# Optimization experiments

Hardware: AMD Instinct MI355X
Metric: run time of the kernel (lower is better)

The kernel has to match this reference:

```python
import jax, jax.numpy as jnp
import numpy as np

N_HEADS = 8
D_EMBED = 1024
D_CROSS = 768
D_HEAD = D_EMBED // N_HEADS  # 128; used only as softmax scale (matches original code)


def setup_inputs() -> dict:
    key = jax.random.key(0)
    ks = jax.random.split(key, 10)
    B, Lq, Lkv = 16, 4096, 77
    s_e = 1.0 / np.sqrt(D_EMBED)
    s_c = 1.0 / np.sqrt(D_CROSS)
    return {
        "x": jax.random.normal(ks[0], (B, Lq, D_EMBED), jnp.float32),
        "y": jax.random.normal(ks[1], (B, Lkv, D_CROSS), jnp.float32),
        "Wq": jax.random.normal(ks[2], (D_EMBED, D_EMBED), jnp.float32) * s_e,
        "bq": jnp.zeros((D_EMBED,), jnp.float32),
        "Wk": jax.random.normal(ks[3], (D_CROSS, D_EMBED), jnp.float32) * s_c,
        "bk": jnp.zeros((D_EMBED,), jnp.float32),
        "Wv": jax.random.normal(ks[4], (D_CROSS, D_EMBED), jnp.float32) * s_c,
        "bv": jnp.zeros((D_EMBED,), jnp.float32),
        "Wo": jax.random.normal(ks[5], (D_EMBED, D_EMBED), jnp.float32) * s_e,
        "bo": jnp.zeros((D_EMBED,), jnp.float32),
    }


def reference(x, y, Wq, bq, Wk, bk, Wv, bv, Wo, bo):
    # Projections
    q = jnp.einsum("bqd,de->bqe", x, Wq) + bq          # [B, Lq, D]
    k = jnp.einsum("bkc,ce->bke", y, Wk) + bk          # [B, Lkv, D]
    v = jnp.einsum("bkc,ce->bke", y, Wv) + bv          # [B, Lkv, D]
    # Original module does NOT split heads; scale uses d_head = d_embed // n_heads
    scale = 1.0 / np.sqrt(D_HEAD)
    scores = jnp.einsum("bqe,bke->bqk", q, k) * scale  # [B, Lq, Lkv]
    attn = jax.nn.softmax(scores, axis=-1)
    out = jnp.einsum("bqk,bke->bqe", attn, v)          # [B, Lq, D]
    return jnp.einsum("bqe,ef->bqf", out, Wo) + bo
```

## Files before the change

### kernel.cpp

```cpp
#include <hip/hip_runtime.h>

typedef unsigned short u16;
typedef __bf16 bf16x8 __attribute__((ext_vector_type(8)));
typedef float f32x4 __attribute__((ext_vector_type(4)));

static __device__ __forceinline__ u16 f2bf(float f) {
  unsigned u = __builtin_bit_cast(unsigned, f);
  u = u + 0x7FFFu + ((u >> 16) & 1u);
  return (u16)(u >> 16);
}
static __device__ __forceinline__ float bf2f(u16 h) {
  return __builtin_bit_cast(float, (unsigned)h << 16);
}

#define GLOAD_LDS16(g, l) __builtin_amdgcn_global_load_lds(              \
    (const __attribute__((address_space(1))) void*)(g),                  \
    (__attribute__((address_space(3))) void*)(l), 16, 0, 0)
#define BAR() asm volatile("s_barrier" ::: "memory")
#define VMCNT(n) asm volatile("s_waitcnt vmcnt(" #n ")" ::: "memory")
#define LGKM0() do { asm volatile("s_waitcnt lgkmcnt(0)" ::: "memory");   \
                     __builtin_amdgcn_sched_barrier(0); } while (0)

__global__ __launch_bounds__(256) void prep(
    const float* __restrict__ Wq, const float* __restrict__ bq,
    const float* __restrict__ Wk, const float* __restrict__ bk,
    const float* __restrict__ Wv, const float* __restrict__ bv,
    const float* __restrict__ Wo, const float* __restrict__ y,
    u16* __restrict__ Wqb, u16* __restrict__ Wkb, u16* __restrict__ Wvb,
    u16* __restrict__ Wot, u16* __restrict__ yp,
    float* __restrict__ zeros, float* __restrict__ bvo,
    float* __restrict__ wkbq, float* __restrict__ bkq) {
  __shared__ float tile[32][33];
  const int blk = blockIdx.x, tid = threadIdx.x;
  if (blk < 4) {
    zeros[blk * 256 + tid] = 0.f;
  } else if (blk < 8) {
    int j = (blk - 4) * 256 + tid;
    float s = 0.f;
    for (int e = 0; e < 1024; ++e) s += bv[e] * Wo[(long)e * 1024 + j];
    bvo[j] = s;
  } else if (blk < 200) {
    int w = (blk - 8) * 4 + (tid >> 6);
    int lane = tid & 63;
    const float* r = Wk + (long)w * 1024;
    float s = 0.f;
#pragma unroll
    for (int i = 0; i < 4; ++i) {
      f32x4 a = *reinterpret_cast<const f32x4*>(r + lane * 4 + i * 256);
      f32x4 b = *reinterpret_cast<const f32x4*>(bq + lane * 4 + i * 256);
      s += a[0] * b[0] + a[1] * b[1] + a[2] * b[2] + a[3] * b[3];
    }
#pragma unroll
    for (int off = 1; off < 64; off <<= 1) s += __shfl_xor(s, off, 64);
    if (lane == 0) wkbq[w] = s;
  } else if (blk < 456) {
    int w = (blk - 200) * 4 + (tid >> 6);
    int lane = tid & 63;
    const float* r = Wq + (long)w * 1024;
    float s = 0.f;
#pragma unroll
    for (int i = 0; i < 4; ++i) {
      f32x4 a = *reinterpret_cast<const f32x4*>(r + lane * 4 + i * 256);
      f32x4 b = *reinterpret_cast<const f32x4*>(bk + lane * 4 + i * 256);
      s += a[0] * b[0] + a[1] * b[1] + a[2] * b[2] + a[3] * b[3];
    }
#pragma unroll
    for (int off = 1; off < 64; off <<= 1) s += __shfl_xor(s, off, 64);
    if (lane == 0) bkq[w] = s;
  } else if (blk < 3016) {
    const float* src; u16* dst; long i;
    if (blk < 1480)      { src = Wq; dst = Wqb; i = (long)(blk - 456) * 256 + tid; }
    else if (blk < 2248) { src = Wk; dst = Wkb; i = (long)(blk - 1480) * 256 + tid; }
    else                 { src = Wv; dst = Wvb; i = (long)(blk - 2248) * 256 + tid; }
    float4 v = reinterpret_cast<const float4*>(src)[i];
    ushort4 o;
    o.x = f2bf(v.x); o.y = f2bf(v.y); o.z = f2bf(v.z); o.w = f2bf(v.w);
    reinterpret_cast<ushort4*>(dst)[i] = o;
  } else if (blk < 4040) {
    int lb = blk - 3016;
    const int tx = tid & 31, ty = tid >> 5;
    const int n0 = (lb & 31) * 32, k0 = (lb >> 5) * 32;
#pragma unroll
    for (int i = 0; i < 4; ++i)
      tile[ty + i * 8][tx] = Wo[(long)(k0 + ty + i * 8) * 1024 + n0 + tx];
    __syncthreads();
#pragma unroll
    for (int i = 0; i < 4; ++i) {
      int r = ty + i * 8;
      Wot[(long)(n0 + r) * 1024 + k0 + tx] = f2bf(tile[tx][r]);
    }
  } else {
    int idx = (blk - 4040) * 256 + tid;
    int e = idx * 4;
    int c = e % 768;
    int rb = e / 768;
    int r = rb % 80, b = rb / 80;
    ushort4 o;
    if (r < 77) {
      float4 v = *reinterpret_cast<const float4*>(y + ((long)(b * 77 + r) * 768 + c));
      o.x = f2bf(v.x); o.y = f2bf(v.y); o.z = f2bf(v.z); o.w = f2bf(v.w);
    } else {
      o.x = 0; o.y = 0; o.z = 0; o.w = 0;
    }
    *reinterpret_cast<ushort4*>(yp + e) = o;
  }
}

static __device__ void gemm_body(int flat, int nb,
                                 const u16* __restrict__ A,
                                 const u16* __restrict__ Bt,
                                 const float* __restrict__ bias,
                                 u16* __restrict__ Cv,
                                 int M, int N, int K) {
  extern __shared__ __align__(16) u16 lds[];
  const int tid = threadIdx.x;
  const int lane = tid & 63, wid = tid >> 6;
  const int lr = lane & 15, lk = lane >> 4;
  const int wr = wid >> 2, wc = wid & 3;

  int widx = flat;
  if ((nb & 7) == 0) {
    int per = nb >> 3;
    widx = (flat & 7) * per + (flat >> 3);
  }
  const int nbx = N >> 8;
  const long m0 = (long)(widx / nbx) * 256;
  const long n0 = (long)(widx % nbx) * 256;
  const int nt = K >> 6;

  f32x4 acc[8][4] = {};

  const long abase = m0 * (long)K;
  const long bbase = n0 * (long)K;
  const int srl = tid >> 3;
  const int scl = tid & 7;

#define STAGE_HALF(SRC, sbase, t_, half_, ldsbase)                           \
  do {                                                                       \
    long k0_ = (long)(t_) * 64;                                              \
    _Pragma("unroll")                                                        \
    for (int j_ = 0; j_ < 2; ++j_) {                                         \
      int row_ = (half_) * 128 + j_ * 64 + srl;                              \
      int cg_ = scl ^ (row_ & 7);                                            \
      GLOAD_LDS16(SRC + (sbase) + (long)row_ * K + k0_ + cg_ * 8,            \
                  lds + (ldsbase) + row_ * 64 + scl * 8);                    \
    }                                                                        \
  } while (0)

#define LDB_ALL(p)                                                           \
  _Pragma("unroll")                                                          \
  for (int n_ = 0; n_ < 4; ++n_)                                             \
    _Pragma("unroll")                                                        \
    for (int kk_ = 0; kk_ < 2; ++kk_) {                                      \
      int row_ = wc * 64 + n_ * 16 + lr;                                     \
      int ch_ = (kk_ * 4 + lk) ^ (lr & 7);                                   \
      bq[n_][kk_] = *reinterpret_cast<const bf16x8*>(                        \
          lds + 32768 + (p) * 16384 + row_ * 64 + ch_ * 8);                  \
    }

#define LDA_Q(p, q)                                                          \
  _Pragma("unroll")                                                          \
  for (int i_ = 0; i_ < 2; ++i_)                                             \
    _Pragma("unroll")                                                        \
    for (int kk_ = 0; kk_ < 2; ++kk_) {                                      \
      int row_ = wr * 128 + ((q) * 2 + i_) * 16 + lr;                        \
      int ch_ = (kk_ * 4 + lk) ^ (lr & 7);                                   \
      af[i_][kk_] = *reinterpret_cast<const bf16x8*>(                        \
          lds + (p) * 16384 + row_ * 64 + ch_ * 8);                          \
    }

#define MFMA_Q(q)                                                            \
  __builtin_amdgcn_s_setprio(1);                                             \
  _Pragma("unroll")                                                          \
  for (int kk_ = 0; kk_ < 2; ++kk_)                                          \
    _Pragma("unroll")                                                        \
    for (int i_ = 0; i_ < 2; ++i_)                                           \
      _Pragma("unroll")                                                      \
      for (int n_ = 0; n_ < 4; ++n_)                                         \
        acc[(q) * 2 + i_][n_] = __builtin_amdgcn_mfma_f32_16x16x32_bf16(     \
            af[i_][kk_], bq[n_][kk_], acc[(q) * 2 + i_][n_], 0, 0, 0);       \
  __builtin_amdgcn_s_setprio(0);

  STAGE_HALF(A, abase, 0, 0, 0);
  STAGE_HALF(A, abase, 0, 1, 0);
  STAGE_HALF(Bt, bbase, 0, 0, 32768);
  STAGE_HALF(Bt, bbase, 0, 1, 32768);
  STAGE_HALF(Bt, bbase, 1, 0, 49152);
  STAGE_HALF(Bt, bbase, 1, 1, 49152);
  VMCNT(4);
  BAR();

  const int niter = nt >> 1;
  for (int tp = 0; tp < niter; ++tp) {
    const int T = tp << 1;
    const bool more = (T + 2 < nt);
    bf16x8 af[2][2], bq[4][2];

    LDB_ALL(0); LDA_Q(0, 0);
    STAGE_HALF(A, abase, T + 1, 0, 16384);
    BAR(); LGKM0(); MFMA_Q(0); BAR();
    LDA_Q(0, 1);
    STAGE_HALF(A, abase, T + 1, 1, 16384);
    BAR(); LGKM0(); MFMA_Q(1); BAR();
    LDA_Q(0, 2);
    if (more) STAGE_HALF(Bt, bbase, T + 2, 0, 32768);
    BAR(); LGKM0(); MFMA_Q(2); BAR();
    LDA_Q(0, 3);
    if (more) { STAGE_HALF(Bt, bbase, T + 2, 1, 32768); VMCNT(4); }
    else VMCNT(0);
    BAR(); LGKM0(); MFMA_Q(3); BAR();

    LDB_ALL(1); LDA_Q(1, 0);
    if (more) STAGE_HALF(A, abase, T + 2, 0, 0);
    BAR(); LGKM0(); MFMA_Q(0); BAR();
    LDA_Q(1, 1);
    if (more) STAGE_HALF(A, abase, T + 2, 1, 0);
    BAR(); LGKM0(); MFMA_Q(1); BAR();
    LDA_Q(1, 2);
    if (more) STAGE_HALF(Bt, bbase, T + 3, 0, 49152);
    BAR(); LGKM0(); MFMA_Q(2); BAR();
    LDA_Q(1, 3);
    if (more) { STAGE_HALF(Bt, bbase, T + 3, 1, 49152); VMCNT(4); }
    BAR(); LGKM0(); MFMA_Q(3); BAR();
  }

  const long mrow = m0 + wr * 128;
  const long ncol = n0 + wc * 64;

  __syncthreads();
  u16* ep = lds + wid * (16 * 72);
  float bb[4];
#pragma unroll
  for (int n = 0; n < 4; ++n) bb[n] = bias[ncol + n * 16 + lr];
  const int rr = lane >> 4, cc = lane & 15;
#pragma unroll
  for (int m = 0; m < 8; ++m) {
#pragma unroll
    for (int n = 0; n < 4; ++n)
#pragma unroll
      for (int j = 0; j < 4; ++j)
        ep[(lk * 4 + j) * 72 + n * 16 + lr] = f2bf(acc[m][n][j] + bb[n]);
    asm volatile("s_waitcnt lgkmcnt(0)" ::: "memory");
#pragma unroll
    for (int s = 0; s < 4; ++s) {
      uint2 v = *reinterpret_cast<const uint2*>(ep + (s * 4 + rr) * 72 + cc * 4);
      *reinterpret_cast<uint2*>(Cv + (mrow + m * 16 + s * 4 + rr) * N +
                                ncol + cc * 4) = v;
    }
    asm volatile("s_waitcnt lgkmcnt(0)" ::: "memory");
  }
#undef STAGE_HALF
#undef LDB_ALL
#undef LDA_Q
#undef MFMA_Q
}

__global__ __launch_bounds__(512, 2) void stageA(
    const u16* Wqb, const u16* Wkb, const u16* Wvb, const u16* Wot,
    const float* zeros, u16* G, u16* WvWoT,
    const u16* yp, const float* wkbq, float* bqk) {
  if (blockIdx.x < 24) {
    if (blockIdx.x < 12)
      gemm_body(blockIdx.x, 12, Wqb, Wkb, zeros, G, 1024, 768, 1024);
    else
      gemm_body(blockIdx.x - 12, 12, Wot, Wvb, zeros, WvWoT, 1024, 768, 1024);
  } else {
    int w = (int)(blockIdx.x - 24) * 8 + ((int)threadIdx.x >> 6);
    int lane = threadIdx.x & 63;
    const u16* r = yp + (long)w * 768;
    float s = 0.f;
#pragma unroll
    for (int i = 0; i < 3; ++i) {
      ushort4 a = *reinterpret_cast<const ushort4*>(r + lane * 4 + i * 256);
      f32x4 b = *reinterpret_cast<const f32x4*>(wkbq + lane * 4 + i * 256);
      s += bf2f(a.x) * b[0] + bf2f(a.y) * b[1] + bf2f(a.z) * b[2] + bf2f(a.w) * b[3];
    }
#pragma unroll
    for (int off = 1; off < 64; off <<= 1) s += __shfl_xor(s, off, 64);
    if (lane == 0) bqk[w] = s;
  }
}

__global__ __launch_bounds__(512, 2) void gemm8_pair(
    int split,
    const u16* A0, const u16* B0, const float* b0, u16* C0, int M0, int N0, int K0,
    const u16* A1, const u16* B1, const float* b1, u16* C1, int M1, int N1, int K1) {
  if ((int)blockIdx.x < split)
    gemm_body(blockIdx.x, split, A0, B0, b0, C0, M0, N0, K0);
  else
    gemm_body(blockIdx.x - split, gridDim.x - split, A1, B1, b1, C1, M1, N1, K1);
}

__global__ __launch_bounds__(256) void packs1(const u16* __restrict__ VWop,
                                              u16* __restrict__ Vt,
                                              const u16* __restrict__ M1T,
                                              u16* __restrict__ M1f) {
  __shared__ u16 tile[32][34];
  const int blk = blockIdx.x, tid = threadIdx.x;
  if (blk < 1536) {
    const int tx = tid & 31, ty = tid >> 5;
    const int e0 = (blk & 31) * 32;
    const int k0 = ((blk >> 5) % 3) * 32;
    const int b = blk / 96;
    const u16* src = VWop + (long)b * 80 * 1024;
#pragma unroll
    for (int i = 0; i < 4; ++i) {
      int k = k0 + ty + i * 8;
      tile[ty + i * 8][tx] = (k < 80) ? src[(long)k * 1024 + e0 + tx] : (u16)0;
    }
    __syncthreads();
    u16* dst = Vt + (long)b * 1024 * 96;
#pragma unroll
    for (int i = 0; i < 4; ++i) {
      int e = e0 + ty + i * 8;
      dst[(long)e * 96 + k0 + tx] = tile[tx][ty + i * 8];
    }
  } else {
    const int lane = tid & 63;
    const int w = (blk - 1536) * 4 + (tid >> 6);
    const int b = w / 160, rem = w % 160;
    const int kk = rem / 5, n = rem % 5;
    const int lr = lane & 15, lk = lane >> 4;
    const u16* src = M1T + ((long)b * 80 + n * 16 + lr) * 1024 + kk * 32 + lk * 8;
    *reinterpret_cast<ulong2*>(M1f + (long)w * 512 + lane * 8) =
        *reinterpret_cast<const ulong2*>(src);
  }
}

__global__ __launch_bounds__(256) void pack_v(const u16* __restrict__ Vt,
                                              u16* __restrict__ Vf) {
  const int lane = threadIdx.x & 63;
  const int w = blockIdx.x * 4 + (threadIdx.x >> 6);
  const int b = w / 192, rem = w % 192;
  const int ct = rem / 3, kk = rem % 3;
  const int lr = lane & 15, lk = lane >> 4;
  const u16* src = Vt + (long)b * 1024 * 96 + (long)(ct * 16 + lr) * 96 + kk * 32 + lk * 8;
  *reinterpret_cast<ulong2*>(Vf + (long)w * 512 + lane * 8) =
      *reinterpret_cast<const ulong2*>(src);
}

__global__ __launch_bounds__(256, 2) void attn_full(const float* __restrict__ x,
                                                    const u16* __restrict__ M1f,
                                                    const float* __restrict__ bqk,
                                                    const u16* __restrict__ VWof,
                                                    const float* __restrict__ bo,
                                                    float* __restrict__ out) {
  extern __shared__ __align__(16) u16 dl[];
  __shared__ __align__(16) u16 P_lds[16][104];
  const long blk = blockIdx.x;
  const int b = (int)(blk >> 8);
  const int tid = threadIdx.x;
  const int lane = tid & 63, wave = tid >> 6;
  const int lr = lane & 15, lk = lane >> 4;
  float* S4 = reinterpret_cast<float*>(dl);
  float* otf = reinterpret_cast<float*>(dl);

  {
    const int row = tid >> 4, cseg = tid & 15;
    const float* src = x + (blk * 16 + row) * 1024 + cseg * 64;
    u16* dst = dl + row * 1032 + cseg * 64;
#pragma unroll
    for (int i = 0; i < 16; ++i) {
      f32x4 v = *reinterpret_cast<const f32x4*>(src + i * 4);
      ushort4 o;
      o.x = f2bf(v[0]); o.y = f2bf(v[1]); o.z = f2bf(v[2]); o.w = f2bf(v[3]);
      *reinterpret_cast<ushort4*>(dst + i * 4) = o;
    }
  }
  __syncthreads();

  f32x4 acc[5] = {};
  const u16* mfb = M1f + (long)b * 81920;
#pragma unroll
  for (int t = 0; t < 8; ++t) {
    int kk = wave * 8 + t;
    bf16x8 qa = *reinterpret_cast<const bf16x8*>(dl + lr * 1032 + kk * 32 + lk * 8);
#pragma unroll
    for (int n = 0; n < 5; ++n) {
      bf16x8 mf = *reinterpret_cast<const bf16x8*>(mfb + ((long)kk * 5 + n) * 512 + lane * 8);
      acc[n] = __builtin_amdgcn_mfma_f32_16x16x32_bf16(qa, mf, acc[n], 0, 0, 0);
    }
  }
  __syncthreads();

#pragma unroll
  for (int n = 0; n < 5; ++n)
#pragma unroll
    for (int j = 0; j < 4; ++j)
      S4[(wave * 16 + lk * 4 + j) * 80 + n * 16 + lr] = acc[n][j];
  __syncthreads();

  {
    const int r = tid >> 4, ci = tid & 15;
    const float scale = 0.088388347648318447f;
    float v[5];
    float mx = -3e38f;
#pragma unroll
    for (int i = 0; i < 5; ++i) {
      int c = ci + 16 * i;
      float s = (S4[r * 80 + c] + S4[(16 + r) * 80 + c]) +
                (S4[(32 + r) * 80 + c] + S4[(48 + r) * 80 + c]);
      s = (s + bqk[b * 80 + c]) * scale;
      if (c >= 77) s = -3e38f;
      v[i] = s;
      mx = fmaxf(mx, s);
    }
#pragma unroll
    for (int off = 1; off < 16; off <<= 1) mx = fmaxf(mx, __shfl_xor(mx, off, 64));
    float sum = 0.f, e[5];
#pragma unroll
    for (int i = 0; i < 5; ++i) { e[i] = __expf(v[i] - mx); sum += e[i]; }
#pragma unroll
    for (int off = 1; off < 16; off <<= 1) sum += __shfl_xor(sum, off, 64);
    float inv = 1.f / sum;
#pragma unroll
    for (int i = 0; i < 5; ++i) P_lds[r][ci + 16 * i] = f2bf(e[i] * inv);
    P_lds[r][80 + ci] = 0;
  }
  __syncthreads();

  bf16x8 pa[3];
#pragma unroll
  for (int kk = 0; kk < 3; ++kk)
    pa[kk] = *reinterpret_cast<const bf16x8*>(&P_lds[lr][kk * 32 + lk * 8]);
  const u16* vfb = VWof + (long)b * 98304;
  float* otw = otf + wave * (16 * 260);
#pragma unroll
  for (int n = 0; n < 16; ++n) {
    int ct = wave * 16 + n;
    f32x4 o = {};
#pragma unroll
    for (int kk = 0; kk < 3; ++kk) {
      bf16x8 vq = *reinterpret_cast<const bf16x8*>(vfb + ((long)ct * 3 + kk) * 512 + lane * 8);
      o = __builtin_amdgcn_mfma_f32_16x16x32_bf16(pa[kk], vq, o, 0, 0, 0);
    }
    float bov = bo[ct * 16 + lr];
#pragma unroll
    for (int j = 0; j < 4; ++j)
      otw[(lk * 4 + j) * 260 + n * 16 + lr] = o[j] + bov;
  }
  __syncthreads();

  float* ob = out + blk * 16384;
#pragma unroll
  for (int rnd = 0; rnd < 16; ++rnd) {
    int off = (rnd * 256 + tid) * 4;
    int row = off >> 10, col = off & 1023;
    int ws = col >> 8, cl = col & 255;
    f32x4 v = *reinterpret_cast<const f32x4*>(otf + ws * (16 * 260) + row * 260 + cl);
    *reinterpret_cast<f32x4*>(ob + off) = v;
  }
}

extern "C" void kernel_launch(void* const* d_in, const int* in_sizes, int n_in,
                              void* d_out, int out_size, void* d_ws, size_t ws_size,
                              hipStream_t stream) {
  const float* x  = (const float*)d_in[0];
  const float* y  = (const float*)d_in[1];
  const float* Wq = (const float*)d_in[2];
  const float* bq = (const float*)d_in[3];
  const float* Wk = (const float*)d_in[4];
  const float* bk = (const float*)d_in[5];
  const float* Wv = (const float*)d_in[6];
  const float* bv = (const float*)d_in[7];
  const float* Wo = (const float*)d_in[8];
  const float* bo = (const float*)d_in[9];

  const int B = 16, D = 1024, Dc = 768, Lp = 80;

  char* p = (char*)d_ws;
  u16* Wqb   = (u16*)p; p += (size_t)D * D * 2;
  u16* Wkb   = (u16*)p; p += (size_t)Dc * D * 2;
  u16* Wvb   = (u16*)p; p += (size_t)Dc * D * 2;
  u16* Wot   = (u16*)p; p += (size_t)D * D * 2;
  u16* yp    = (u16*)p; p += (size_t)B * Lp * Dc * 2;
  u16* G     = (u16*)p; p += (size_t)D * Dc * 2;
  u16* WvWoT = (u16*)p; p += (size_t)D * Dc * 2;
  u16* M1T   = (u16*)p; p += (size_t)B * Lp * D * 2;
  u16* VWop  = (u16*)p; p += (size_t)B * Lp * D * 2;
  u16* Vt    = (u16*)p; p += (size_t)B * D * 96 * 2;
  u16* VWof  = (u16*)p; p += (size_t)B * 64 * 3 * 512 * 2;
  u16* M1f   = (u16*)p; p += (size_t)B * 160 * 512 * 2;
  float* zeros = (float*)p; p += (size_t)1024 * 4;
  float* bvoB  = (float*)p; p += (size_t)1024 * 4;
  float* wkbq  = (float*)p; p += (size_t)768 * 4;
  float* bkqB  = (float*)p; p += (size_t)1024 * 4;
  float* bqkB  = (float*)p; p += (size_t)1280 * 4;

  (void)hipFuncSetAttribute(reinterpret_cast<const void*>(&stageA),
                            hipFuncAttributeMaxDynamicSharedMemorySize, 131072);
  (void)hipFuncSetAttribute(reinterpret_cast<const void*>(&gemm8_pair),
                            hipFuncAttributeMaxDynamicSharedMemorySize, 131072);
  (void)hipFuncSetAttribute(reinterpret_cast<const void*>(&attn_full),
                            hipFuncAttributeMaxDynamicSharedMemorySize, 66560);

  prep<<<5000, 256, 0, stream>>>(Wq, bq, Wk, bk, Wv, bv, Wo, y,
                                 Wqb, Wkb, Wvb, Wot, yp,
                                 zeros, bvoB, wkbq, bkqB);

  stageA<<<184, 512, 131072, stream>>>(Wqb, Wkb, Wvb, Wot, zeros, G, WvWoT,
                                       yp, wkbq, bqkB);

  gemm8_pair<<<40, 512, 131072, stream>>>(
      20,
      yp, G, bkqB, M1T, B * Lp, D, Dc,
      yp, WvWoT, bvoB, VWop, B * Lp, D, Dc);

  packs1<<<2176, 256, 0, stream>>>(VWop, Vt, M1T, M1f);
  pack_v<<<768, 256, 0, stream>>>(Vt, VWof);

  attn_full<<<4096, 256, 66560, stream>>>(x, M1f, bqkB, VWof, bo, (float*)d_out);
}
```

Before: 285.3 us.

## Halve attn_full LDS footprint with fragment-ordered x tile and streamed output

The x tile is now stored in LDS directly in MFMA fragment order (padded 520-element blocks) with coalesced row-wise global loads. The output stage is split into four groups per wave, each staged through a small per-wave 16x68 buffer and written straight to global memory, instead of a full 16x1024 fp32 staging area behind a block-wide barrier. This cuts dynamic LDS from 66560 to 33280 bytes and raises launch bounds to 4 blocks per CU, aiming for higher occupancy and better latency hiding. The cost is extra per-wave waitcnt syncs and narrower 256-byte global write segments per row.

```diff
diff --git a/kernel.cpp b/kernel.cpp
--- a/kernel.cpp
+++ b/kernel.cpp
@@ -339,7 +339,7 @@
       *reinterpret_cast<const ulong2*>(src);
 }
 
-__global__ __launch_bounds__(256, 2) void attn_full(const float* __restrict__ x,
+__global__ __launch_bounds__(256, 4) void attn_full(const float* __restrict__ x,
                                                     const u16* __restrict__ M1f,
                                                     const float* __restrict__ bqk,
                                                     const u16* __restrict__ VWof,
@@ -353,18 +353,17 @@
   const int lane = tid & 63, wave = tid >> 6;
   const int lr = lane & 15, lk = lane >> 4;
   float* S4 = reinterpret_cast<float*>(dl);
-  float* otf = reinterpret_cast<float*>(dl);
 
   {
-    const int row = tid >> 4, cseg = tid & 15;
-    const float* src = x + (blk * 16 + row) * 1024 + cseg * 64;
-    u16* dst = dl + row * 1032 + cseg * 64;
-#pragma unroll
-    for (int i = 0; i < 16; ++i) {
-      f32x4 v = *reinterpret_cast<const f32x4*>(src + i * 4);
+    const float* xb = x + blk * 16384;
+#pragma unroll
+    for (int r = 0; r < 16; ++r) {
+      f32x4 v = *reinterpret_cast<const f32x4*>(xb + r * 1024 + tid * 4);
       ushort4 o;
       o.x = f2bf(v[0]); o.y = f2bf(v[1]); o.z = f2bf(v[2]); o.w = f2bf(v[3]);
-      *reinterpret_cast<ushort4*>(dst + i * 4) = o;
+      int c = tid * 4;
+      int kk = c >> 5, lkx = (c >> 3) & 3, e = c & 7;
+      *reinterpret_cast<ushort4*>(dl + kk * 520 + (lkx * 16 + r) * 8 + e) = o;
     }
   }
   __syncthreads();
@@ -374,7 +373,7 @@
 #pragma unroll
   for (int t = 0; t < 8; ++t) {
     int kk = wave * 8 + t;
-    bf16x8 qa = *reinterpret_cast<const bf16x8*>(dl + lr * 1032 + kk * 32 + lk * 8);
+    bf16x8 qa = *reinterpret_cast<const bf16x8*>(dl + kk * 520 + lane * 8);
 #pragma unroll
     for (int n = 0; n < 5; ++n) {
       bf16x8 mf = *reinterpret_cast<const bf16x8*>(mfb + ((long)kk * 5 + n) * 512 + lane * 8);
@@ -424,31 +423,33 @@
   for (int kk = 0; kk < 3; ++kk)
     pa[kk] = *reinterpret_cast<const bf16x8*>(&P_lds[lr][kk * 32 + lk * 8]);
   const u16* vfb = VWof + (long)b * 98304;
-  float* otw = otf + wave * (16 * 260);
-#pragma unroll
-  for (int n = 0; n < 16; ++n) {
-    int ct = wave * 16 + n;
-    f32x4 o = {};
-#pragma unroll
-    for (int kk = 0; kk < 3; ++kk) {
-      bf16x8 vq = *reinterpret_cast<const bf16x8*>(vfb + ((long)ct * 3 + kk) * 512 + lane * 8);
-      o = __builtin_amdgcn_mfma_f32_16x16x32_bf16(pa[kk], vq, o, 0, 0, 0);
-    }
-    float bov = bo[ct * 16 + lr];
-#pragma unroll
-    for (int j = 0; j < 4; ++j)
-      otw[(lk * 4 + j) * 260 + n * 16 + lr] = o[j] + bov;
-  }
-  __syncthreads();
-
+  float* otw = reinterpret_cast<float*>(dl) + wave * (16 * 68);
   float* ob = out + blk * 16384;
-#pragma unroll
-  for (int rnd = 0; rnd < 16; ++rnd) {
-    int off = (rnd * 256 + tid) * 4;
-    int row = off >> 10, col = off & 1023;
-    int ws = col >> 8, cl = col & 255;
-    f32x4 v = *reinterpret_cast<const f32x4*>(otf + ws * (16 * 260) + row * 260 + cl);
-    *reinterpret_cast<f32x4*>(ob + off) = v;
+  const int rr = lane >> 4, cc = lane & 15;
+#pragma unroll
+  for (int grp = 0; grp < 4; ++grp) {
+#pragma unroll
+    for (int n = 0; n < 4; ++n) {
+      int ct = wave * 16 + grp * 4 + n;
+      f32x4 o = {};
+#pragma unroll
+      for (int kk = 0; kk < 3; ++kk) {
+        bf16x8 vq = *reinterpret_cast<const bf16x8*>(vfb + ((long)ct * 3 + kk) * 512 + lane * 8);
+        o = __builtin_amdgcn_mfma_f32_16x16x32_bf16(pa[kk], vq, o, 0, 0, 0);
+      }
+      float bov = bo[ct * 16 + lr];
+#pragma unroll
+      for (int j = 0; j < 4; ++j)
+        otw[(lk * 4 + j) * 68 + n * 16 + lr] = o[j] + bov;
+    }
+    asm volatile("s_waitcnt lgkmcnt(0)" ::: "memory");
+#pragma unroll
+    for (int s = 0; s < 4; ++s) {
+      f32x4 v = *reinterpret_cast<const f32x4*>(otw + (s * 4 + rr) * 68 + cc * 4);
+      *reinterpret_cast<f32x4*>(ob + (s * 4 + rr) * 1024 + wave * 256 +
+                                grp * 64 + cc * 4) = v;
+    }
+    asm volatile("s_waitcnt lgkmcnt(0)" ::: "memory");
   }
 }
 
@@ -492,7 +493,7 @@
   (void)hipFuncSetAttribute(reinterpret_cast<const void*>(&gemm8_pair),
                             hipFuncAttributeMaxDynamicSharedMemorySize, 131072);
   (void)hipFuncSetAttribute(reinterpret_cast<const void*>(&attn_full),
-                            hipFuncAttributeMaxDynamicSharedMemorySize, 66560);
+                            hipFuncAttributeMaxDynamicSharedMemorySize, 33280);
 
   prep<<<5000, 256, 0, stream>>>(Wq, bq, Wk, bk, Wv, bv, Wo, y,
                                  Wqb, Wkb, Wvb, Wot, yp,
@@ -509,5 +510,5 @@
   packs1<<<2176, 256, 0, stream>>>(VWop, Vt, M1T, M1f);
   pack_v<<<768, 256, 0, stream>>>(Vt, VWof);
 
-  attn_full<<<4096, 256, 66560, stream>>>(x, M1f, bqkB, VWof, bo, (float*)d_out);
-}
+  attn_full<<<4096, 256, 33280, stream>>>(x, M1f, bqkB, VWof, bo, (float*)d_out);
+}
```

New measurement: 252.4 us. -11.5%, faster.
